# Kernel tuning notes

Hardware: AMD Instinct MI355X
Metric: run time of the kernel (lower is better)

Reference implementation:

```python
import jax, jax.numpy as jnp
import numpy as np

N1, N2, N3 = 40000, 30000, 30000
N = N1 + N2 + N3          # total nodes after vstack
E = 800000                # edges
D_IN = 256                # in_channels
D_HID = 256               # 2 * out_channels
D_OUT = 128               # out_channels


def _glorot(k, shape):
    lim = (6.0 / (shape[0] + shape[1])) ** 0.5
    return jax.random.uniform(k, shape, jnp.float32, -lim, lim)


def setup_inputs() -> dict:
    key = jax.random.key(0)
    ks = jax.random.split(key, 12)
    x1 = jax.random.normal(ks[0], (N1, 128), jnp.float32)
    x2 = jax.random.normal(ks[1], (N2, 256), jnp.float32)
    x3 = jax.random.normal(ks[2], (N3, 64), jnp.float32)
    edge_index = jax.random.randint(ks[3], (2, E), 0, N, jnp.int64)
    return {
        "x1": x1, "x2": x2, "x3": x3,
        "Wp1": _glorot(ks[4], (128, D_IN)), "bp1": jnp.zeros((D_IN,), jnp.float32),
        "Wp2": _glorot(ks[5], (256, D_IN)), "bp2": jnp.zeros((D_IN,), jnp.float32),
        "Wp3": _glorot(ks[6], (64, D_IN)),  "bp3": jnp.zeros((D_IN,), jnp.float32),
        "W1": _glorot(ks[7], (D_IN, D_HID)), "b1": jnp.zeros((D_HID,), jnp.float32),
        "W2": _glorot(ks[8], (D_HID, D_OUT)), "b2": jnp.zeros((D_OUT,), jnp.float32),
        "edge_index": edge_index,
    }


def _gcn_conv(x, W, b, src, dst, dis):
    # PyG GCNConv: h = xW; out[j] = sum_i norm_ij * h[i] (incl. self-loop) + b
    h = x @ W                                   # [N, d_out]
    msg = h[src] * (dis[src] * dis[dst])[:, None]   # [E, d_out] edge messages
    agg = jax.ops.segment_sum(msg, dst, num_segments=N)
    agg = agg + h * (dis * dis)[:, None]        # self-loop term (norm = 1/deg)
    return agg + b


def reference(x1, x2, x3, Wp1, bp1, Wp2, bp2, Wp3, bp3, W1, b1, W2, b2, edge_index):
    # per-type projection + vstack
    x = jnp.concatenate([x1 @ Wp1 + bp1, x2 @ Wp2 + bp2, x3 @ Wp3 + bp3], axis=0)
    # dropout(p=0.5) is identity in eval mode (deterministic baseline)
    src, dst = edge_index[0], edge_index[1]
    # degree with self-loops (in-degree at dst, as in PyG gcn_norm)
    deg = jnp.ones((N,), x.dtype).at[dst].add(1.0)
    dis = jax.lax.rsqrt(deg)                    # deg^{-1/2}
    h = jax.nn.relu(_gcn_conv(x, W1, b1, src, dst, dis))
    return _gcn_conv(h, W2, b2, src, dst, dis)
```

## Files before the change

kernel.cpp:

```cpp
#include <hip/hip_runtime.h>
#include <cstddef>

#define NT 100000
#define NN1 40000
#define NN2 30000
#define NN3 30000
#define EE 800000
#define DIN 256
#define DHID 256
#define DOUT 128

typedef _Float16 f16;
typedef f16 f16x8 __attribute__((ext_vector_type(8)));
typedef f16 f16x4 __attribute__((ext_vector_type(4)));
typedef float f32x4 __attribute__((ext_vector_type(4)));

static inline int cdiv(int a, int b) { return (a + b - 1) / b; }

__device__ __forceinline__ void gload_lds16(const f16* g, f16* l) {
    __builtin_amdgcn_global_load_lds(
        (const __attribute__((address_space(1))) void*)g,
        (__attribute__((address_space(3))) void*)l, 16, 0, 0);
}

__global__ void k_hist(const int* __restrict__ dst, int* __restrict__ cnt, int e) {
    int i = blockIdx.x * blockDim.x + threadIdx.x;
    if (i < e) atomicAdd(&cnt[dst[i]], 1);
}

__global__ void k_scan1(const int* __restrict__ cnt, int* __restrict__ rowptr,
                        int* __restrict__ part, float* __restrict__ dis, int n) {
    __shared__ int sums[256];
    int b = blockIdx.x, t = threadIdx.x;
    int base = b * 1024 + t * 4;
    int v0 = (base + 0 < n) ? cnt[base + 0] : 0;
    int v1 = (base + 1 < n) ? cnt[base + 1] : 0;
    int v2 = (base + 2 < n) ? cnt[base + 2] : 0;
    int v3 = (base + 3 < n) ? cnt[base + 3] : 0;
    if (base + 0 < n) dis[base + 0] = rsqrtf((float)v0 + 1.0f);
    if (base + 1 < n) dis[base + 1] = rsqrtf((float)v1 + 1.0f);
    if (base + 2 < n) dis[base + 2] = rsqrtf((float)v2 + 1.0f);
    if (base + 3 < n) dis[base + 3] = rsqrtf((float)v3 + 1.0f);
    int tsum = v0 + v1 + v2 + v3;
    sums[t] = tsum;
    __syncthreads();
    for (int off = 1; off < 256; off <<= 1) {
        int y = (t >= off) ? sums[t - off] : 0;
        __syncthreads();
        sums[t] += y;
        __syncthreads();
    }
    int excl = sums[t] - tsum;
    if (base + 0 < n) rowptr[base + 0] = excl;
    if (base + 1 < n) rowptr[base + 1] = excl + v0;
    if (base + 2 < n) rowptr[base + 2] = excl + v0 + v1;
    if (base + 3 < n) rowptr[base + 3] = excl + v0 + v1 + v2;
    if (t == 255) part[b] = sums[255];
}

__global__ void k_scan2(int* __restrict__ part, int nb) {
    __shared__ int sums[256];
    int t = threadIdx.x;
    int v = (t < nb) ? part[t] : 0;
    sums[t] = v;
    __syncthreads();
    for (int off = 1; off < 256; off <<= 1) {
        int y = (t >= off) ? sums[t - off] : 0;
        __syncthreads();
        sums[t] += y;
        __syncthreads();
    }
    if (t < nb) part[t] = sums[t] - v;
}

__global__ void k_scan3(int* __restrict__ rowptr, const int* __restrict__ part,
                        int n, int total) {
    int i = blockIdx.x * blockDim.x + threadIdx.x;
    if (i < n) rowptr[i] += part[i >> 10];
    if (i == 0) rowptr[n] = total;
}

__global__ void k_fill(const int* __restrict__ src, const int* __restrict__ dst,
                       const float* __restrict__ dis, const int* __restrict__ rowptr,
                       int* __restrict__ cursor, int2* __restrict__ e_pairs, int e) {
    int i = blockIdx.x * blockDim.x + threadIdx.x;
    if (i >= e) return;
    int s = src[i], t = dst[i];
    int pos = atomicAdd(&cursor[t], 1);
    int2 p;
    p.x = s;
    p.y = __float_as_int(dis[s] * dis[t]);
    e_pairs[rowptr[t] + pos] = p;
}

__global__ void k_cvt_all(const float* __restrict__ a, int na4,
                          const float* __restrict__ b, int nb4,
                          const float* __restrict__ c, int nc4,
                          f16* __restrict__ o) {
    int i = blockIdx.x * blockDim.x + threadIdx.x;
    const float* s; int j;
    if (i < na4) { s = a; j = i; }
    else if (i < na4 + nb4) { s = b; j = i - na4; }
    else if (i < na4 + nb4 + nc4) { s = c; j = i - na4 - nb4; }
    else return;
    float4 v = reinterpret_cast<const float4*>(s)[j];
    f16x4 r = {(f16)v.x, (f16)v.y, (f16)v.z, (f16)v.w};
    reinterpret_cast<f16x4*>(o)[i] = r;
}

struct TArgs {
    const float *W0, *W1, *W2, *W3, *W4;
    f16 *T0, *T1, *T2, *T3, *T4;
};
__global__ void k_transpose_all(TArgs t) {
    int i = blockIdx.x * blockDim.x + threadIdx.x;
    const float* W; f16* T; int K, N, j;
    if      (i <  32768) { W = t.W0; T = t.T0; K = 128; N = 256; j = i; }
    else if (i <  98304) { W = t.W1; T = t.T1; K = 256; N = 256; j = i - 32768; }
    else if (i < 114688) { W = t.W2; T = t.T2; K =  64; N = 256; j = i - 98304; }
    else if (i < 180224) { W = t.W3; T = t.T3; K = 256; N = 256; j = i - 114688; }
    else if (i < 212992) { W = t.W4; T = t.T4; K = 256; N = 128; j = i - 180224; }
    else return;
    int k = j / N, n = j - k * N;
    T[n * K + k] = (f16)W[j];
}

template<bool RELU_OUT, bool HAS_BIAS>
__device__ __forceinline__
void hgemm_body(f16* As, f16* Bs,
                const f16* __restrict__ A, const f16* __restrict__ BT,
                const float* __restrict__ bias, f16* __restrict__ C,
                int M, int K, int N, int bx, int by) {
    const int tid = threadIdx.x;
    const int lane = tid & 63;
    const int wid = tid >> 6;
    const int wm = wid & 1, wn = wid >> 1;
    const int bm = bx * 128;
    const int bn = by * 128;
    const int r15 = lane & 15, g = lane >> 4;
    const int sr  = lane >> 2;
    const int chs = (lane & 3) ^ ((lane >> 3) & 3);

    auto stage = [&](int buf, int k0) {
        #pragma unroll
        for (int q = 0; q < 2; ++q) {
            int chunk = wid + q * 4;
            int row = chunk * 16 + sr;
            int ga = bm + row; if (ga >= M) ga = M - 1;
            gload_lds16(A  + (size_t)ga * K + k0 + chs * 8, As + buf * 4096 + chunk * 512);
            gload_lds16(BT + (size_t)(bn + row) * K + k0 + chs * 8, Bs + buf * 4096 + chunk * 512);
        }
    };

    f32x4 acc[4][4] = {};
    const int nsteps = K >> 5;
    stage(0, 0);
    __syncthreads();
    int cur = 0;
    for (int step = 0; step < nsteps; ++step) {
        if (step + 1 < nsteps) stage(cur ^ 1, (step + 1) << 5);
        f16x8 af[4], bf[4];
        const int sl = (g ^ ((r15 >> 1) & 3)) * 8;
        #pragma unroll
        for (int mf = 0; mf < 4; ++mf) {
            int row = wm * 64 + mf * 16 + r15;
            af[mf] = *reinterpret_cast<const f16x8*>(As + cur * 4096 + row * 32 + sl);
        }
        #pragma unroll
        for (int nf = 0; nf < 4; ++nf) {
            int row = wn * 64 + nf * 16 + r15;
            bf[nf] = *reinterpret_cast<const f16x8*>(Bs + cur * 4096 + row * 32 + sl);
        }
        #pragma unroll
        for (int mf = 0; mf < 4; ++mf)
            #pragma unroll
            for (int nf = 0; nf < 4; ++nf)
                acc[mf][nf] = __builtin_amdgcn_mfma_f32_16x16x32_f16(af[mf], bf[nf], acc[mf][nf], 0, 0, 0);
        __syncthreads();
        cur ^= 1;
    }

    #pragma unroll
    for (int mf = 0; mf < 4; ++mf) {
        #pragma unroll
        for (int nf = 0; nf < 4; ++nf) {
            int col = bn + wn * 64 + nf * 16 + r15;
            float bv = HAS_BIAS ? bias[col] : 0.f;
            #pragma unroll
            for (int r = 0; r < 4; ++r) {
                int rowg = bm + wm * 64 + mf * 16 + g * 4 + r;
                if (rowg < M) {
                    float v = acc[mf][nf][r] + bv;
                    if (RELU_OUT) v = fmaxf(v, 0.f);
                    C[(size_t)rowg * N + col] = (f16)v;
                }
            }
        }
    }
}

template<bool RELU_OUT, bool HAS_BIAS>
__global__ __launch_bounds__(256)
void k_hgemm(const f16* __restrict__ A, const f16* __restrict__ BT,
             const float* __restrict__ bias, f16* __restrict__ C,
             int M, int K, int N) {
    extern __shared__ f16 smem[];
    hgemm_body<RELU_OUT, HAS_BIAS>(smem, smem + 8192, A, BT, bias, C, M, K, N,
                                   blockIdx.x, blockIdx.y);
}

struct P3 {
    const f16 *a1, *a2, *a3, *t1, *t2, *t3;
    const float *b1, *b2, *b3;
    f16 *o1, *o2, *o3;
    int g1, g2;
};
__global__ __launch_bounds__(256) void k_proj3(P3 p) {
    extern __shared__ f16 smem[];
    int bx = blockIdx.x, by = blockIdx.y;
    if (bx < p.g1)
        hgemm_body<false, true>(smem, smem + 8192, p.a1, p.t1, p.b1, p.o1, NN1, 128, 256, bx, by);
    else if (bx < p.g1 + p.g2)
        hgemm_body<false, true>(smem, smem + 8192, p.a2, p.t2, p.b2, p.o2, NN2, 256, 256, bx - p.g1, by);
    else
        hgemm_body<false, true>(smem, smem + 8192, p.a3, p.t3, p.b3, p.o3, NN3, 64, 256, bx - p.g1 - p.g2, by);
}

__global__ void k_gather256(const f16* __restrict__ f, const float* __restrict__ dis,
                            const int* __restrict__ rowptr, const int2* __restrict__ e_pairs,
                            f16* __restrict__ outb, int n) {
    int node = (int)(((long long)blockIdx.x * blockDim.x + threadIdx.x) >> 5);
    int l = threadIdx.x & 31;
    if (node >= n) return;
    float dj = dis[node];
    int r0 = rowptr[node], r1 = rowptr[node + 1];
    int deg = r1 - r0;
    int si = 0; float wi = 0.f;
    if (l < deg) { int2 p = e_pairs[r0 + l]; si = p.x; wi = __int_as_float(p.y); }
    f16x8 a = reinterpret_cast<const f16x8*>(f + (size_t)node * 256)[l];
    float ws = dj * dj;
    float acc[8];
    #pragma unroll
    for (int k = 0; k < 8; ++k) acc[k] = (float)a[k] * ws;
    int n32 = deg < 32 ? deg : 32;
    int e = 0;
    for (; e + 4 <= n32; e += 4) {
        int s0 = __shfl(si, e + 0, 32), s1 = __shfl(si, e + 1, 32);
        int s2 = __shfl(si, e + 2, 32), s3 = __shfl(si, e + 3, 32);
        float w0 = __shfl(wi, e + 0, 32), w1 = __shfl(wi, e + 1, 32);
        float w2 = __shfl(wi, e + 2, 32), w3 = __shfl(wi, e + 3, 32);
        f16x8 u0 = reinterpret_cast<const f16x8*>(f + (size_t)s0 * 256)[l];
        f16x8 u1 = reinterpret_cast<const f16x8*>(f + (size_t)s1 * 256)[l];
        f16x8 u2 = reinterpret_cast<const f16x8*>(f + (size_t)s2 * 256)[l];
        f16x8 u3 = reinterpret_cast<const f16x8*>(f + (size_t)s3 * 256)[l];
        #pragma unroll
        for (int k = 0; k < 8; ++k)
            acc[k] += (float)u0[k] * w0 + (float)u1[k] * w1 + (float)u2[k] * w2 + (float)u3[k] * w3;
    }
    for (; e < n32; ++e) {
        int s0 = __shfl(si, e, 32);
        float w0 = __shfl(wi, e, 32);
        f16x8 u0 = reinterpret_cast<const f16x8*>(f + (size_t)s0 * 256)[l];
        #pragma unroll
        for (int k = 0; k < 8; ++k) acc[k] += (float)u0[k] * w0;
    }
    for (int e2 = r0 + 32; e2 < r1; ++e2) {
        int2 p = e_pairs[e2];
        float w0 = __int_as_float(p.y);
        f16x8 u0 = reinterpret_cast<const f16x8*>(f + (size_t)p.x * 256)[l];
        #pragma unroll
        for (int k = 0; k < 8; ++k) acc[k] += (float)u0[k] * w0;
    }
    f16x8 r;
    #pragma unroll
    for (int k = 0; k < 8; ++k) r[k] = (f16)acc[k];
    reinterpret_cast<f16x8*>(outb + (size_t)node * 256)[l] = r;
}

__global__ void k_gather128(const f16* __restrict__ f, const float* __restrict__ dis,
                            const int* __restrict__ rowptr, const int2* __restrict__ e_pairs,
                            const float* __restrict__ bias, float* __restrict__ outb, int n) {
    int node = (int)(((long long)blockIdx.x * blockDim.x + threadIdx.x) >> 5);
    int l = threadIdx.x & 31;
    if (node >= n) return;
    float dj = dis[node];
    int r0 = rowptr[node], r1 = rowptr[node + 1];
    int deg = r1 - r0;
    int si = 0; float wi = 0.f;
    if (l < deg) { int2 p = e_pairs[r0 + l]; si = p.x; wi = __int_as_float(p.y); }
    f16x4 a = reinterpret_cast<const f16x4*>(f + (size_t)node * 128)[l];
    float ws = dj * dj;
    float acc[4];
    #pragma unroll
    for (int k = 0; k < 4; ++k) acc[k] = (float)a[k] * ws;
    int n32 = deg < 32 ? deg : 32;
    int e = 0;
    for (; e + 4 <= n32; e += 4) {
        int s0 = __shfl(si, e + 0, 32), s1 = __shfl(si, e + 1, 32);
        int s2 = __shfl(si, e + 2, 32), s3 = __shfl(si, e + 3, 32);
        float w0 = __shfl(wi, e + 0, 32), w1 = __shfl(wi, e + 1, 32);
        float w2 = __shfl(wi, e + 2, 32), w3 = __shfl(wi, e + 3, 32);
        f16x4 u0 = reinterpret_cast<const f16x4*>(f + (size_t)s0 * 128)[l];
        f16x4 u1 = reinterpret_cast<const f16x4*>(f + (size_t)s1 * 128)[l];
        f16x4 u2 = reinterpret_cast<const f16x4*>(f + (size_t)s2 * 128)[l];
        f16x4 u3 = reinterpret_cast<const f16x4*>(f + (size_t)s3 * 128)[l];
        #pragma unroll
        for (int k = 0; k < 4; ++k)
            acc[k] += (float)u0[k] * w0 + (float)u1[k] * w1 + (float)u2[k] * w2 + (float)u3[k] * w3;
    }
    for (; e < n32; ++e) {
        int s0 = __shfl(si, e, 32);
        float w0 = __shfl(wi, e, 32);
        f16x4 u0 = reinterpret_cast<const f16x4*>(f + (size_t)s0 * 128)[l];
        #pragma unroll
        for (int k = 0; k < 4; ++k) acc[k] += (float)u0[k] * w0;
    }
    for (int e2 = r0 + 32; e2 < r1; ++e2) {
        int2 p = e_pairs[e2];
        float w0 = __int_as_float(p.y);
        f16x4 u0 = reinterpret_cast<const f16x4*>(f + (size_t)p.x * 128)[l];
        #pragma unroll
        for (int k = 0; k < 4; ++k) acc[k] += (float)u0[k] * w0;
    }
    float4 bb = reinterpret_cast<const float4*>(bias)[l];
    float4 r = make_float4(acc[0] + bb.x, acc[1] + bb.y, acc[2] + bb.z, acc[3] + bb.w);
    reinterpret_cast<float4*>(outb + (size_t)node * 128)[l] = r;
}

extern "C" void kernel_launch(void* const* d_in, const int* in_sizes, int n_in,
                              void* d_out, int out_size, void* d_ws, size_t ws_size,
                              hipStream_t stream) {
    const float* x1  = (const float*)d_in[0];
    const float* x2  = (const float*)d_in[1];
    const float* x3  = (const float*)d_in[2];
    const float* Wp1 = (const float*)d_in[3];
    const float* bp1 = (const float*)d_in[4];
    const float* Wp2 = (const float*)d_in[5];
    const float* bp2 = (const float*)d_in[6];
    const float* Wp3 = (const float*)d_in[7];
    const float* bp3 = (const float*)d_in[8];
    const float* W1  = (const float*)d_in[9];
    const float* b1  = (const float*)d_in[10];
    const float* W2  = (const float*)d_in[11];
    const float* b2  = (const float*)d_in[12];
    const int*   ei  = (const int*)d_in[13];
    const int* src = ei;
    const int* dst = ei + EE;
    float* out = (float*)d_out;

    char* ws = (char*)d_ws;
    size_t off = 0;
    auto alloc = [&](size_t bytes) {
        char* p = ws + off;
        off += (bytes + 511) & ~(size_t)511;
        return p;
    };
    float* dis    = (float*)alloc((size_t)NT * 4);
    int*   cnt    = (int*)alloc((size_t)NT * 4);
    int*   cursor = (int*)alloc((size_t)NT * 4);
    int*   rowptr = (int*)alloc((size_t)(NT + 1) * 4);
    int*   part   = (int*)alloc(256 * 4);
    int2*  e_pairs= (int2*)alloc((size_t)EE * 8);
    f16*   slotX  = (f16*)alloc((size_t)NT * 256 * 2);
    f16*   slotY  = (f16*)alloc((size_t)NT * 256 * 2);
    f16*   xc     = (f16*)alloc((size_t)(NN1 * 128 + NN2 * 256 + NN3 * 64) * 2);
    f16*   Wp1T   = (f16*)alloc((size_t)256 * 128 * 2);
    f16*   Wp2T   = (f16*)alloc((size_t)256 * 256 * 2);
    f16*   Wp3T   = (f16*)alloc((size_t)256 * 64 * 2);
    f16*   W1T    = (f16*)alloc((size_t)256 * 256 * 2);
    f16*   W2T    = (f16*)alloc((size_t)128 * 256 * 2);

    f16* x1c = xc;
    f16* x2c = xc + (size_t)NN1 * 128;
    f16* x3c = xc + (size_t)NN1 * 128 + (size_t)NN2 * 256;
    f16* x16   = slotX;
    f16* agg16 = slotY;
    f16* h16   = slotX;
    f16* hw216 = slotY;

    const int nb = cdiv(NT, 1024);

    size_t zspan = (size_t)((char*)rowptr - (char*)cnt);
    hipMemsetAsync(cnt, 0, zspan, stream);
    k_hist<<<cdiv(EE, 256), 256, 0, stream>>>(dst, cnt, EE);
    k_scan1<<<nb, 256, 0, stream>>>(cnt, rowptr, part, dis, NT);
    k_scan2<<<1, 256, 0, stream>>>(part, nb);
    k_scan3<<<cdiv(NT, 256), 256, 0, stream>>>(rowptr, part, NT, EE);
    k_fill<<<cdiv(EE, 256), 256, 0, stream>>>(src, dst, dis, rowptr, cursor, e_pairs, EE);

    {
        int na4 = NN1 * 128 / 4, nb4 = NN2 * 256 / 4, nc4 = NN3 * 64 / 4;
        k_cvt_all<<<cdiv(na4 + nb4 + nc4, 256), 256, 0, stream>>>(x1, na4, x2, nb4, x3, nc4, xc);
        TArgs t = {Wp1, Wp2, Wp3, W1, W2, Wp1T, Wp2T, Wp3T, W1T, W2T};
        k_transpose_all<<<cdiv(212992, 256), 256, 0, stream>>>(t);
    }

    {
        P3 p = {x1c, x2c, x3c, Wp1T, Wp2T, Wp3T, bp1, bp2, bp3,
                x16, x16 + (size_t)NN1 * 256, x16 + (size_t)(NN1 + NN2) * 256,
                cdiv(NN1, 128), cdiv(NN2, 128)};
        dim3 g(cdiv(NN1, 128) + cdiv(NN2, 128) + cdiv(NN3, 128), 2);
        k_proj3<<<g, 256, 32768, stream>>>(p);
    }

    k_gather256<<<cdiv(NT * 32, 256), 256, 0, stream>>>(x16, dis, rowptr, e_pairs, agg16, NT);

    {
        dim3 g(cdiv(NT, 128), 2);
        k_hgemm<true, true><<<g, 256, 32768, stream>>>(agg16, W1T, b1, h16, NT, 256, 256);
    }

    {
        dim3 g(cdiv(NT, 128), 1);
        k_hgemm<false, false><<<g, 256, 32768, stream>>>(h16, W2T, nullptr, hw216, NT, 256, 128);
    }

    k_gather128<<<cdiv(NT * 32, 256), 256, 0, stream>>>(hw216, dis, rowptr, e_pairs, b2, out, NT);
}
```

Measured before the change: 313.4 us.

## Fuse layer-1 gather, W1 GEMM with ReLU, and W2 GEMM into one kernel

Replaces the separate 256-wide gather kernel and two hgemm launches with a single kernel. Each block aggregates 64 nodes into a swizzled LDS tile, runs the W1 MFMA GEMM with bias and ReLU back into the same LDS tile, then runs the W2 GEMM and writes hw2. This removes global round-trips for the aggregated features and the hidden activations, plus two launches. In exchange the B operands are loaded straight from global memory without LDS staging, and the gather phase's latency now sits inside a block that also does GEMM work, so occupancy and latency hiding may suffer.

```diff
diff --git a/kernel.cpp b/kernel.cpp
--- a/kernel.cpp
+++ b/kernel.cpp
@@ -6,9 +6,6 @@
 #define NN2 30000
 #define NN3 30000
 #define EE 800000
-#define DIN 256
-#define DHID 256
-#define DOUT 128
 
 typedef _Float16 f16;
 typedef f16 f16x8 __attribute__((ext_vector_type(8)));
@@ -199,16 +196,6 @@
     }
 }
 
-template<bool RELU_OUT, bool HAS_BIAS>
-__global__ __launch_bounds__(256)
-void k_hgemm(const f16* __restrict__ A, const f16* __restrict__ BT,
-             const float* __restrict__ bias, f16* __restrict__ C,
-             int M, int K, int N) {
-    extern __shared__ f16 smem[];
-    hgemm_body<RELU_OUT, HAS_BIAS>(smem, smem + 8192, A, BT, bias, C, M, K, N,
-                                   blockIdx.x, blockIdx.y);
-}
-
 struct P3 {
     const f16 *a1, *a2, *a3, *t1, *t2, *t3;
     const float *b1, *b2, *b3;
@@ -226,55 +213,152 @@
         hgemm_body<false, true>(smem, smem + 8192, p.a3, p.t3, p.b3, p.o3, NN3, 64, 256, bx - p.g1 - p.g2, by);
 }
 
-__global__ void k_gather256(const f16* __restrict__ f, const float* __restrict__ dis,
-                            const int* __restrict__ rowptr, const int2* __restrict__ e_pairs,
-                            f16* __restrict__ outb, int n) {
-    int node = (int)(((long long)blockIdx.x * blockDim.x + threadIdx.x) >> 5);
-    int l = threadIdx.x & 31;
-    if (node >= n) return;
-    float dj = dis[node];
-    int r0 = rowptr[node], r1 = rowptr[node + 1];
-    int deg = r1 - r0;
-    int si = 0; float wi = 0.f;
-    if (l < deg) { int2 p = e_pairs[r0 + l]; si = p.x; wi = __int_as_float(p.y); }
-    f16x8 a = reinterpret_cast<const f16x8*>(f + (size_t)node * 256)[l];
-    float ws = dj * dj;
-    float acc[8];
+__global__ __launch_bounds__(256)
+void k_fused(const f16* __restrict__ x16, const float* __restrict__ dis,
+             const int* __restrict__ rowptr, const int2* __restrict__ e_pairs,
+             const f16* __restrict__ W1T, const float* __restrict__ b1,
+             const f16* __restrict__ W2T, f16* __restrict__ hw2, int M) {
+    __shared__ f16 P[64 * 256];
+    const int tid = threadIdx.x;
+    const int lane = tid & 63;
+    const int bm = blockIdx.x * 64;
+
+    {
+        const int grp = tid >> 5;
+        const int l = tid & 31;
+        for (int it = 0; it < 8; ++it) {
+            int row = it * 8 + grp;
+            int node = bm + row;
+            float av[8];
+            if (node < M) {
+                float dj = dis[node];
+                int r0 = rowptr[node], r1 = rowptr[node + 1];
+                int deg = r1 - r0;
+                int si = 0; float wi = 0.f;
+                if (l < deg) { int2 pr = e_pairs[r0 + l]; si = pr.x; wi = __int_as_float(pr.y); }
+                f16x8 a = reinterpret_cast<const f16x8*>(x16 + (size_t)node * 256)[l];
+                float wself = dj * dj;
+                #pragma unroll
+                for (int k = 0; k < 8; ++k) av[k] = (float)a[k] * wself;
+                int n32 = deg < 32 ? deg : 32;
+                int e = 0;
+                for (; e + 4 <= n32; e += 4) {
+                    int s0 = __shfl(si, e + 0, 32), s1 = __shfl(si, e + 1, 32);
+                    int s2 = __shfl(si, e + 2, 32), s3 = __shfl(si, e + 3, 32);
+                    float w0 = __shfl(wi, e + 0, 32), w1 = __shfl(wi, e + 1, 32);
+                    float w2 = __shfl(wi, e + 2, 32), w3 = __shfl(wi, e + 3, 32);
+                    f16x8 u0 = reinterpret_cast<const f16x8*>(x16 + (size_t)s0 * 256)[l];
+                    f16x8 u1 = reinterpret_cast<const f16x8*>(x16 + (size_t)s1 * 256)[l];
+                    f16x8 u2 = reinterpret_cast<const f16x8*>(x16 + (size_t)s2 * 256)[l];
+                    f16x8 u3 = reinterpret_cast<const f16x8*>(x16 + (size_t)s3 * 256)[l];
+                    #pragma unroll
+                    for (int k = 0; k < 8; ++k)
+                        av[k] += (float)u0[k] * w0 + (float)u1[k] * w1
+                               + (float)u2[k] * w2 + (float)u3[k] * w3;
+                }
+                for (; e < n32; ++e) {
+                    int s0 = __shfl(si, e, 32);
+                    float w0 = __shfl(wi, e, 32);
+                    f16x8 u0 = reinterpret_cast<const f16x8*>(x16 + (size_t)s0 * 256)[l];
+                    #pragma unroll
+                    for (int k = 0; k < 8; ++k) av[k] += (float)u0[k] * w0;
+                }
+                for (int e2 = r0 + 32; e2 < r1; ++e2) {
+                    int2 pr = e_pairs[e2];
+                    float w0 = __int_as_float(pr.y);
+                    f16x8 u0 = reinterpret_cast<const f16x8*>(x16 + (size_t)pr.x * 256)[l];
+                    #pragma unroll
+                    for (int k = 0; k < 8; ++k) av[k] += (float)u0[k] * w0;
+                }
+            } else {
+                #pragma unroll
+                for (int k = 0; k < 8; ++k) av[k] = 0.f;
+            }
+            f16x8 r;
+            #pragma unroll
+            for (int k = 0; k < 8; ++k) r[k] = (f16)av[k];
+            int slot = (l & 3) ^ ((row >> 1) & 3);
+            *reinterpret_cast<f16x8*>(P + (l >> 2) * 2048 + row * 32 + slot * 8) = r;
+        }
+    }
+    __syncthreads();
+
+    const int wn = tid >> 6;
+    const int r15 = lane & 15, g = lane >> 4;
+    f32x4 acc[4][4] = {};
+    for (int step = 0; step < 8; ++step) {
+        f16x8 af[4], bf[4];
+        #pragma unroll
+        for (int mf = 0; mf < 4; ++mf) {
+            int row = mf * 16 + r15;
+            int slot = g ^ ((row >> 1) & 3);
+            af[mf] = *reinterpret_cast<const f16x8*>(P + step * 2048 + row * 32 + slot * 8);
+        }
+        #pragma unroll
+        for (int nf = 0; nf < 4; ++nf) {
+            int n1 = wn * 64 + nf * 16 + r15;
+            bf[nf] = *reinterpret_cast<const f16x8*>(W1T + (size_t)n1 * 256 + step * 32 + g * 8);
+        }
+        #pragma unroll
+        for (int mf = 0; mf < 4; ++mf)
+            #pragma unroll
+            for (int nf = 0; nf < 4; ++nf)
+                acc[mf][nf] = __builtin_amdgcn_mfma_f32_16x16x32_f16(af[mf], bf[nf], acc[mf][nf], 0, 0, 0);
+    }
+    __syncthreads();
+
     #pragma unroll
-    for (int k = 0; k < 8; ++k) acc[k] = (float)a[k] * ws;
-    int n32 = deg < 32 ? deg : 32;
-    int e = 0;
-    for (; e + 4 <= n32; e += 4) {
-        int s0 = __shfl(si, e + 0, 32), s1 = __shfl(si, e + 1, 32);
-        int s2 = __shfl(si, e + 2, 32), s3 = __shfl(si, e + 3, 32);
-        float w0 = __shfl(wi, e + 0, 32), w1 = __shfl(wi, e + 1, 32);
-        float w2 = __shfl(wi, e + 2, 32), w3 = __shfl(wi, e + 3, 32);
-        f16x8 u0 = reinterpret_cast<const f16x8*>(f + (size_t)s0 * 256)[l];
-        f16x8 u1 = reinterpret_cast<const f16x8*>(f + (size_t)s1 * 256)[l];
-        f16x8 u2 = reinterpret_cast<const f16x8*>(f + (size_t)s2 * 256)[l];
-        f16x8 u3 = reinterpret_cast<const f16x8*>(f + (size_t)s3 * 256)[l];
-        #pragma unroll
-        for (int k = 0; k < 8; ++k)
-            acc[k] += (float)u0[k] * w0 + (float)u1[k] * w1 + (float)u2[k] * w2 + (float)u3[k] * w3;
-    }
-    for (; e < n32; ++e) {
-        int s0 = __shfl(si, e, 32);
-        float w0 = __shfl(wi, e, 32);
-        f16x8 u0 = reinterpret_cast<const f16x8*>(f + (size_t)s0 * 256)[l];
-        #pragma unroll
-        for (int k = 0; k < 8; ++k) acc[k] += (float)u0[k] * w0;
-    }
-    for (int e2 = r0 + 32; e2 < r1; ++e2) {
-        int2 p = e_pairs[e2];
-        float w0 = __int_as_float(p.y);
-        f16x8 u0 = reinterpret_cast<const f16x8*>(f + (size_t)p.x * 256)[l];
-        #pragma unroll
-        for (int k = 0; k < 8; ++k) acc[k] += (float)u0[k] * w0;
-    }
-    f16x8 r;
+    for (int nf = 0; nf < 4; ++nf) {
+        int col = wn * 64 + nf * 16 + r15;
+        float bv = b1[col];
+        int s = col >> 5, gp = (col >> 3) & 3, c7 = col & 7;
+        #pragma unroll
+        for (int mf = 0; mf < 4; ++mf) {
+            #pragma unroll
+            for (int rr = 0; rr < 4; ++rr) {
+                int row = mf * 16 + g * 4 + rr;
+                float v = fmaxf(acc[mf][nf][rr] + bv, 0.f);
+                int slot = gp ^ ((row >> 1) & 3);
+                P[s * 2048 + row * 32 + slot * 8 + c7] = (f16)v;
+            }
+        }
+    }
+    __syncthreads();
+
+    f32x4 acc2[4][2] = {};
+    for (int step = 0; step < 8; ++step) {
+        f16x8 af[4], bf[2];
+        #pragma unroll
+        for (int mf = 0; mf < 4; ++mf) {
+            int row = mf * 16 + r15;
+            int slot = g ^ ((row >> 1) & 3);
+            af[mf] = *reinterpret_cast<const f16x8*>(P + step * 2048 + row * 32 + slot * 8);
+        }
+        #pragma unroll
+        for (int nf = 0; nf < 2; ++nf) {
+            int n2 = wn * 32 + nf * 16 + r15;
+            bf[nf] = *reinterpret_cast<const f16x8*>(W2T + (size_t)n2 * 256 + step * 32 + g * 8);
+        }
+        #pragma unroll
+        for (int mf = 0; mf < 4; ++mf)
+            #pragma unroll
+            for (int nf = 0; nf < 2; ++nf)
+                acc2[mf][nf] = __builtin_amdgcn_mfma_f32_16x16x32_f16(af[mf], bf[nf], acc2[mf][nf], 0, 0, 0);
+    }
+
     #pragma unroll
-    for (int k = 0; k < 8; ++k) r[k] = (f16)acc[k];
-    reinterpret_cast<f16x8*>(outb + (size_t)node * 256)[l] = r;
+    for (int mf = 0; mf < 4; ++mf) {
+        #pragma unroll
+        for (int nf = 0; nf < 2; ++nf) {
+            int col = wn * 32 + nf * 16 + r15;
+            #pragma unroll
+            for (int rr = 0; rr < 4; ++rr) {
+                int rowg = bm + mf * 16 + g * 4 + rr;
+                if (rowg < M)
+                    hw2[(size_t)rowg * 128 + col] = (f16)acc2[mf][nf][rr];
+            }
+        }
+    }
 }
 
 __global__ void k_gather128(const f16* __restrict__ f, const float* __restrict__ dis,
@@ -289,10 +373,10 @@
     int si = 0; float wi = 0.f;
     if (l < deg) { int2 p = e_pairs[r0 + l]; si = p.x; wi = __int_as_float(p.y); }
     f16x4 a = reinterpret_cast<const f16x4*>(f + (size_t)node * 128)[l];
-    float ws = dj * dj;
+    float wsf = dj * dj;
     float acc[4];
     #pragma unroll
-    for (int k = 0; k < 4; ++k) acc[k] = (float)a[k] * ws;
+    for (int k = 0; k < 4; ++k) acc[k] = (float)a[k] * wsf;
     int n32 = deg < 32 ? deg : 32;
     int e = 0;
     for (; e + 4 <= n32; e += 4) {
@@ -361,8 +445,8 @@
     int*   rowptr = (int*)alloc((size_t)(NT + 1) * 4);
     int*   part   = (int*)alloc(256 * 4);
     int2*  e_pairs= (int2*)alloc((size_t)EE * 8);
-    f16*   slotX  = (f16*)alloc((size_t)NT * 256 * 2);
-    f16*   slotY  = (f16*)alloc((size_t)NT * 256 * 2);
+    f16*   x16    = (f16*)alloc((size_t)NT * 256 * 2);
+    f16*   hw216  = (f16*)alloc((size_t)NT * 128 * 2);
     f16*   xc     = (f16*)alloc((size_t)(NN1 * 128 + NN2 * 256 + NN3 * 64) * 2);
     f16*   Wp1T   = (f16*)alloc((size_t)256 * 128 * 2);
     f16*   Wp2T   = (f16*)alloc((size_t)256 * 256 * 2);
@@ -373,10 +457,6 @@
     f16* x1c = xc;
     f16* x2c = xc + (size_t)NN1 * 128;
     f16* x3c = xc + (size_t)NN1 * 128 + (size_t)NN2 * 256;
-    f16* x16   = slotX;
-    f16* agg16 = slotY;
-    f16* h16   = slotX;
-    f16* hw216 = slotY;
 
     const int nb = cdiv(NT, 1024);
 
@@ -403,17 +483,8 @@
         k_proj3<<<g, 256, 32768, stream>>>(p);
     }
 
-    k_gather256<<<cdiv(NT * 32, 256), 256, 0, stream>>>(x16, dis, rowptr, e_pairs, agg16, NT);
-
-    {
-        dim3 g(cdiv(NT, 128), 2);
-        k_hgemm<true, true><<<g, 256, 32768, stream>>>(agg16, W1T, b1, h16, NT, 256, 256);
-    }
-
-    {
-        dim3 g(cdiv(NT, 128), 1);
-        k_hgemm<false, false><<<g, 256, 32768, stream>>>(h16, W2T, nullptr, hw216, NT, 256, 128);
-    }
+    k_fused<<<cdiv(NT, 64), 256, 0, stream>>>(x16, dis, rowptr, e_pairs,
+                                              W1T, b1, W2T, hw216, NT);
 
     k_gather128<<<cdiv(NT * 32, 256), 256, 0, stream>>>(hw216, dis, rowptr, e_pairs, b2, out, NT);
 }
```

Measured after the change: 309.8 us. No clear change (-1.1%).
